# Optimization experiments

Measured on AMD Instinct MI355X. Metric: run time of the kernel, lower is better.

The kernel has to match this reference:

```python
import jax, jax.numpy as jnp
import numpy as np

D_IN = 1024
D_OUT = 1024
NUM_HEADS = 16
HEAD_DIM = D_OUT // NUM_HEADS


def setup_inputs() -> dict:
    key = jax.random.key(0)
    ks = jax.random.split(key, 6)
    s = 1.0 / np.sqrt(D_IN)
    inputs = jax.random.normal(ks[0], (4, 2048, D_IN), dtype=jnp.float32)
    Wq = jax.random.uniform(ks[1], (D_IN, D_OUT), jnp.float32, -s, s)
    Wk = jax.random.uniform(ks[2], (D_IN, D_OUT), jnp.float32, -s, s)
    Wv = jax.random.uniform(ks[3], (D_IN, D_OUT), jnp.float32, -s, s)
    so = 1.0 / np.sqrt(D_OUT)
    Wo = jax.random.uniform(ks[4], (D_OUT, D_OUT), jnp.float32, -so, so)
    bo = jax.random.uniform(ks[5], (D_OUT,), jnp.float32, -so, so)
    return {"inputs": inputs, "Wq": Wq, "Wk": Wk, "Wv": Wv, "Wo": Wo, "bo": bo}


def reference(inputs, Wq, Wk, Wv, Wo, bo):
    b, n, _ = inputs.shape
    # projections -> [b, h, n, d]
    def split_heads(x):
        return x.reshape(b, n, NUM_HEADS, HEAD_DIM).transpose(0, 2, 1, 3)
    q = split_heads(inputs @ Wq)
    k = split_heads(inputs @ Wk)
    v = split_heads(inputs @ Wv)
    scores = jnp.einsum('bhqd,bhkd->bhqk', q, k) / np.sqrt(HEAD_DIM).astype(np.float32)
    causal = jnp.tril(jnp.ones((n, n), dtype=bool))  # True = keep
    scores = jnp.where(causal, scores, -jnp.inf)
    weights = jax.nn.softmax(scores, axis=-1)
    ctx = jnp.einsum('bhqk,bhkd->bhqd', weights, v)
    ctx = ctx.transpose(0, 2, 1, 3).reshape(b, n, D_OUT)
    return ctx @ Wo + bo
```

## Files before the change

kernel.cpp:

```cpp
#include <hip/hip_runtime.h>

typedef unsigned short u16;
typedef unsigned int u32;
typedef __attribute__((ext_vector_type(8))) short short8;
typedef __attribute__((ext_vector_type(4))) float floatx4;
typedef __attribute__((ext_vector_type(4))) unsigned short ushort4_t;
typedef __attribute__((ext_vector_type(4))) float float4_t;
typedef __attribute__((ext_vector_type(2))) unsigned int uint2_t;


__device__ __forceinline__ u16 f2bf(float f) {
  unsigned u = __builtin_bit_cast(unsigned, f);
  u += 0x7FFFu + ((u >> 16) & 1u);
  return (u16)(u >> 16);
}

__device__ __forceinline__ u32 pack_bf2(float a, float b) {
  u32 ua = __builtin_bit_cast(u32, a) + 0x8000u;
  u32 ub = __builtin_bit_cast(u32, b) + 0x8000u;
  return __builtin_amdgcn_perm(ua, ub, 0x07060302u);
}

__device__ __forceinline__ void gload_lds16(const void* g, void* l) {
  __builtin_amdgcn_global_load_lds(
      (const __attribute__((address_space(1))) void*)g,
      (__attribute__((address_space(3))) void*)l, 16, 0, 0);
}


__global__ void cvt_x(const float* __restrict__ src, u16* __restrict__ dst) {
  int i = blockIdx.x * 256 + threadIdx.x;
  float4_t f = ((const float4_t*)src)[i];
  ushort4_t u;
  u.x = f2bf(f.x); u.y = f2bf(f.y); u.z = f2bf(f.z); u.w = f2bf(f.w);
  ((ushort4_t*)dst)[i] = u;
}

__global__ void transpose_cvt4(const float* __restrict__ wq, const float* __restrict__ wk,
                               const float* __restrict__ wv, const float* __restrict__ wo,
                               u16* __restrict__ qk, u16* __restrict__ vt,
                               u16* __restrict__ ot, float sc) {
  int i = blockIdx.x * 256 + threadIdx.x;
  int n = i >> 10, k = i & 1023;
  int which = blockIdx.y;
  const float* s = (which == 0) ? wq : (which == 1) ? wk : (which == 2) ? wv : wo;
  u16* d = (which == 0) ? qk : (which == 1) ? (qk + (1u << 20)) : (which == 2) ? vt : ot;
  float f = s[k * 1024 + n] * ((which == 0) ? sc : 1.f);
  d[i] = f2bf(f);
}

template <int MODE>
__global__ __launch_bounds__(256) void gemm_bt(
    const u16* __restrict__ A, const u16* __restrict__ Bt, void* __restrict__ Cv,
    const float* __restrict__ bias, int K, int lda, int ldb, int ldc) {
  __shared__ u16 As[128 * 32];
  __shared__ u16 Bs[128 * 32];
  const int tid = threadIdx.x;
  const int w = tid >> 6, l = tid & 63, quad = l >> 4, l16 = l & 15;
  const int wm = w >> 1, wn = w & 1;
  const size_t m0 = (size_t)blockIdx.y * 128, n0 = (size_t)blockIdx.x * 128;

  floatx4 acc[4][4];
  for (int i = 0; i < 4; ++i)
    for (int j = 0; j < 4; ++j) acc[i][j] = (floatx4){0.f, 0.f, 0.f, 0.f};

  for (int k0 = 0; k0 < K; k0 += 32) {
    __syncthreads();
    for (int i = 0; i < 2; ++i) {
      int c = i * 256 + tid;
      int row = c >> 2, off = (c & 3) * 8;
      gload_lds16(A + (m0 + row) * (size_t)lda + k0 + off, &As[c * 8]);
      gload_lds16(Bt + (n0 + row) * (size_t)ldb + k0 + off, &Bs[c * 8]);
    }
    __syncthreads();

    short8 a[4], bb[4];
    for (int im = 0; im < 4; ++im)
      a[im] = *(const short8*)&As[(wm * 64 + im * 16 + l16) * 32 + quad * 8];
    for (int in = 0; in < 4; ++in)
      bb[in] = *(const short8*)&Bs[(wn * 64 + in * 16 + l16) * 32 + quad * 8];
    for (int im = 0; im < 4; ++im)
      for (int in = 0; in < 4; ++in)
        acc[im][in] = __builtin_amdgcn_mfma_f32_16x16x32_bf16(a[im], bb[in], acc[im][in], 0, 0, 0);
  }

  for (int im = 0; im < 4; ++im)
    for (int in = 0; in < 4; ++in) {
      size_t r0 = m0 + wm * 64 + im * 16 + quad * 4;
      size_t col = n0 + wn * 64 + in * 16 + l16;
      float bv = (MODE == 1) ? bias[col] : 0.f;
      for (int r = 0; r < 4; ++r) {
        float val = acc[im][in][r] + bv;
        if (MODE == 0)
          ((u16*)Cv)[(r0 + r) * (size_t)ldc + col] = f2bf(val);
        else
          ((float*)Cv)[(r0 + r) * (size_t)ldc + col] = val;
      }
    }
}

__global__ __launch_bounds__(256) void flash_attn(
    const u16* __restrict__ QK, const u16* __restrict__ Vt, u16* __restrict__ ctx) {
  __shared__ u16 Ks[64 * 64];
  __shared__ u16 Vs[64 * 64];
  __shared__ u16 Ps[4 * 16 * 64];
  __shared__ float Ls[4 * 32];

  const int tid = threadIdx.x;
  const int w = tid >> 6, l = tid & 63, quad = l >> 4, l16 = l & 15;
  const int bh = blockIdx.x, qt = 15 - (int)blockIdx.y;
  const int b = bh >> 4, h = bh & 15;
  const int q0w = qt * 128 + w * 32;
  const int nkt = 2 * qt + 2;
  const int xr = (l16 & 7) << 4;

  short8 aq[2][2];
  for (int qf = 0; qf < 2; ++qf) {
    const size_t base = (size_t)(b * 2048 + q0w + qf * 16 + l16) * 2048 + h * 64 + quad * 8;
    aq[qf][0] = *(const short8*)(QK + base);
    aq[qf][1] = *(const short8*)(QK + base + 32);
  }

  floatx4 o[2][4];
  float lsum[2] = {0.f, 0.f};
  for (int qf = 0; qf < 2; ++qf)
    for (int df = 0; df < 4; ++df) o[qf][df] = (floatx4){0.f, 0.f, 0.f, 0.f};

  char* Psw = (char*)Ps + w * 2048;

  for (int kt = 0; kt < nkt; ++kt) {
    __syncthreads();
    for (int i = 0; i < 2; ++i) {
      int c = i * 256 + tid;
      int row = c >> 3, scol = ((c & 7) ^ (row & 7)) << 3;
      gload_lds16(QK + (size_t)(b * 2048 + kt * 64 + row) * 2048 + 1024 + h * 64 + scol,
                  &Ks[c * 8]);
      gload_lds16(Vt + (size_t)(h * 64 + row) * 8192 + b * 2048 + kt * 64 + scol,
                  &Vs[c * 8]);
    }
    __syncthreads();

    if (kt * 64 > q0w + 31) continue;
    const bool need_mask = (kt * 64 + 63) > q0w;

    short8 ka[4][2];
    for (int nf = 0; nf < 4; ++nf) {
      const char* kb = (const char*)Ks + (nf * 16 + l16) * 128;
      ka[nf][0] = *(const short8*)(kb + ((quad * 16) ^ xr));
      ka[nf][1] = *(const short8*)(kb + ((64 + quad * 16) ^ xr));
    }

    for (int qf = 0; qf < 2; ++qf) {
      floatx4 s[4];
      for (int nf = 0; nf < 4; ++nf) s[nf] = (floatx4){0.f, 0.f, 0.f, 0.f};
      for (int nf = 0; nf < 4; ++nf) {
        s[nf] = __builtin_amdgcn_mfma_f32_16x16x32_bf16(ka[nf][0], aq[qf][0], s[nf], 0, 0, 0);
        s[nf] = __builtin_amdgcn_mfma_f32_16x16x32_bf16(ka[nf][1], aq[qf][1], s[nf], 0, 0, 0);
      }
      if (need_mask) {
        int qpos = q0w + qf * 16 + l16;
        for (int nf = 0; nf < 4; ++nf)
          for (int r = 0; r < 4; ++r) {
            int kpos = kt * 64 + nf * 16 + quad * 4 + r;
            if (kpos > qpos) s[nf][r] = -1e30f;
          }
      }
      for (int nf = 0; nf < 4; ++nf) {
        float p0 = __builtin_amdgcn_exp2f(s[nf][0]);
        float p1 = __builtin_amdgcn_exp2f(s[nf][1]);
        float p2 = __builtin_amdgcn_exp2f(s[nf][2]);
        float p3 = __builtin_amdgcn_exp2f(s[nf][3]);
        lsum[qf] += (p0 + p1) + (p2 + p3);
        uint2_t pk;
        pk.x = pack_bf2(p1, p0);
        pk.y = pack_bf2(p3, p2);
        *(uint2_t*)(Psw + l16 * 128 + ((nf * 32 + quad * 8) ^ xr)) = pk;
      }
      for (int kk = 0; kk < 2; ++kk) {
        short8 ap = *(const short8*)(Psw + l16 * 128 + ((kk * 64 + quad * 16) ^ xr));
        for (int df = 0; df < 4; ++df) {
          const char* vb = (const char*)Vs + (df * 16 + l16) * 128;
          short8 bv = *(const short8*)(vb + ((kk * 64 + quad * 16) ^ xr));
          o[qf][df] = __builtin_amdgcn_mfma_f32_16x16x32_bf16(ap, bv, o[qf][df], 0, 0, 0);
        }
      }
    }
  }

  for (int qf = 0; qf < 2; ++qf) {
    float t = lsum[qf];
    t += __shfl_xor(t, 16, 64);
    t += __shfl_xor(t, 32, 64);
    if (l < 16) Ls[w * 32 + qf * 16 + l16] = __builtin_amdgcn_rcpf(t);
  }
  for (int qf = 0; qf < 2; ++qf) {
    floatx4 inv = *(const floatx4*)&Ls[w * 32 + qf * 16 + quad * 4];
    for (int df = 0; df < 4; ++df)
      for (int r = 0; r < 4; ++r) {
        float val = o[qf][df][r] * inv[r];
        size_t row = (size_t)(b * 2048 + q0w + qf * 16 + quad * 4 + r);
        ctx[row * 1024 + h * 64 + df * 16 + l16] = f2bf(val);
      }
  }
}


extern "C" void kernel_launch(void* const* d_in, const int* in_sizes, int n_in,
                              void* d_out, int out_size, void* d_ws, size_t ws_size,
                              hipStream_t stream) {
  const float* X  = (const float*)d_in[0];
  const float* Wq = (const float*)d_in[1];
  const float* Wk = (const float*)d_in[2];
  const float* Wv = (const float*)d_in[3];
  const float* Wo = (const float*)d_in[4];
  const float* bo = (const float*)d_in[5];

  char* ws = (char*)d_ws;
  u16* Xb   = (u16*)(ws);
  u16* WqkT = (u16*)(ws + (16u << 20));
  u16* WvT  = (u16*)(ws + (20u << 20));
  u16* WoT  = (u16*)(ws + (22u << 20));
  u16* QKb  = (u16*)(ws + (24u << 20));
  u16* Vt   = (u16*)(ws + (56u << 20));

  const float SC = 0.125f * 1.44269504088896340736f;

  cvt_x<<<8192, 256, 0, stream>>>(X, Xb);
  transpose_cvt4<<<dim3(4096, 4), 256, 0, stream>>>(Wq, Wk, Wv, Wo, WqkT, WvT, WoT, SC);

  gemm_bt<0><<<dim3(16, 64), 256, 0, stream>>>(Xb, WqkT, QKb, nullptr, 1024, 1024, 1024, 2048);
  gemm_bt<0><<<dim3(64, 8), 256, 0, stream>>>(WvT, Xb, Vt, nullptr, 1024, 1024, 1024, 8192);

  flash_attn<<<dim3(64, 16), 256, 0, stream>>>(QKb, Vt, Xb);

  gemm_bt<1><<<dim3(8, 64), 256, 0, stream>>>(Xb, WoT, (float*)d_out, bo, 1024, 1024, 1024, 1024);
}
```

Before: 287.5 us.

## Double-buffer LDS in GEMM and flash attention, tile weight transpose via shared memory

The GEMM and flash-attention kernels now use two LDS buffers, so the global-to-LDS load for the next K tile is issued before computing on the current one, with a single barrier per iteration. This overlaps memory latency with MFMA work. Flash attention also hoists all V fragment reads ahead of the qf loop and simplifies the masking test. The weight transpose now goes through a padded 64x65 shared tile so that both the global reads and writes are coalesced. The cost is twice the LDS footprint, which may lower occupancy, and more registers for the hoisted V fragments.

New measurement: 268.8 us. -6.5%, faster.

```diff
diff --git a/kernel.cpp b/kernel.cpp
--- a/kernel.cpp
+++ b/kernel.cpp
@@ -36,25 +36,34 @@
   ((ushort4_t*)dst)[i] = u;
 }
 
-__global__ void transpose_cvt4(const float* __restrict__ wq, const float* __restrict__ wk,
-                               const float* __restrict__ wv, const float* __restrict__ wo,
-                               u16* __restrict__ qk, u16* __restrict__ vt,
-                               u16* __restrict__ ot, float sc) {
-  int i = blockIdx.x * 256 + threadIdx.x;
-  int n = i >> 10, k = i & 1023;
-  int which = blockIdx.y;
+__global__ __launch_bounds__(256) void transpose_cvt4(
+    const float* __restrict__ wq, const float* __restrict__ wk,
+    const float* __restrict__ wv, const float* __restrict__ wo,
+    u16* __restrict__ qk, u16* __restrict__ vt, u16* __restrict__ ot, float sc) {
+  __shared__ float T[64][65];
+  const int which = blockIdx.z;
   const float* s = (which == 0) ? wq : (which == 1) ? wk : (which == 2) ? wv : wo;
   u16* d = (which == 0) ? qk : (which == 1) ? (qk + (1u << 20)) : (which == 2) ? vt : ot;
-  float f = s[k * 1024 + n] * ((which == 0) ? sc : 1.f);
-  d[i] = f2bf(f);
+  const float scale = (which == 0) ? sc : 1.f;
+  const int n0 = blockIdx.x * 64, k0 = blockIdx.y * 64;
+  const int c = threadIdx.x & 63, rg = threadIdx.x >> 6;
+  for (int i = 0; i < 16; ++i) {
+    int r = i * 4 + rg;
+    T[r][c] = s[(k0 + r) * 1024 + n0 + c];
+  }
+  __syncthreads();
+  for (int i = 0; i < 16; ++i) {
+    int r = i * 4 + rg;
+    d[(n0 + r) * 1024 + k0 + c] = f2bf(T[c][r] * scale);
+  }
 }
 
 template <int MODE>
 __global__ __launch_bounds__(256) void gemm_bt(
     const u16* __restrict__ A, const u16* __restrict__ Bt, void* __restrict__ Cv,
     const float* __restrict__ bias, int K, int lda, int ldb, int ldc) {
-  __shared__ u16 As[128 * 32];
-  __shared__ u16 Bs[128 * 32];
+  __shared__ u16 As[2][128 * 32];
+  __shared__ u16 Bs[2][128 * 32];
   const int tid = threadIdx.x;
   const int w = tid >> 6, l = tid & 63, quad = l >> 4, l16 = l & 15;
   const int wm = w >> 1, wn = w & 1;
@@ -64,24 +73,33 @@
   for (int i = 0; i < 4; ++i)
     for (int j = 0; j < 4; ++j) acc[i][j] = (floatx4){0.f, 0.f, 0.f, 0.f};
 
-  for (int k0 = 0; k0 < K; k0 += 32) {
-    __syncthreads();
+  auto stage = [&](int k0, int buf) {
     for (int i = 0; i < 2; ++i) {
       int c = i * 256 + tid;
       int row = c >> 2, off = (c & 3) * 8;
-      gload_lds16(A + (m0 + row) * (size_t)lda + k0 + off, &As[c * 8]);
-      gload_lds16(Bt + (n0 + row) * (size_t)ldb + k0 + off, &Bs[c * 8]);
-    }
-    __syncthreads();
+      gload_lds16(A + (m0 + row) * (size_t)lda + k0 + off, &As[buf][c * 8]);
+      gload_lds16(Bt + (n0 + row) * (size_t)ldb + k0 + off, &Bs[buf][c * 8]);
+    }
+  };
+
+  const int nk = K >> 5;
+  stage(0, 0);
+  __syncthreads();
+
+  for (int ki = 0; ki < nk; ++ki) {
+    const int buf = ki & 1;
+    if (ki + 1 < nk) stage((ki + 1) << 5, buf ^ 1);
 
     short8 a[4], bb[4];
     for (int im = 0; im < 4; ++im)
-      a[im] = *(const short8*)&As[(wm * 64 + im * 16 + l16) * 32 + quad * 8];
+      a[im] = *(const short8*)&As[buf][(wm * 64 + im * 16 + l16) * 32 + quad * 8];
     for (int in = 0; in < 4; ++in)
-      bb[in] = *(const short8*)&Bs[(wn * 64 + in * 16 + l16) * 32 + quad * 8];
+      bb[in] = *(const short8*)&Bs[buf][(wn * 64 + in * 16 + l16) * 32 + quad * 8];
     for (int im = 0; im < 4; ++im)
       for (int in = 0; in < 4; ++in)
         acc[im][in] = __builtin_amdgcn_mfma_f32_16x16x32_bf16(a[im], bb[in], acc[im][in], 0, 0, 0);
+
+    __syncthreads();
   }
 
   for (int im = 0; im < 4; ++im)
@@ -101,10 +119,10 @@
 
 __global__ __launch_bounds__(256) void flash_attn(
     const u16* __restrict__ QK, const u16* __restrict__ Vt, u16* __restrict__ ctx) {
-  __shared__ u16 Ks[64 * 64];
-  __shared__ u16 Vs[64 * 64];
+  __shared__ u16 Ks[2][64 * 64];
+  __shared__ u16 Vs[2][64 * 64];
   __shared__ u16 Ps[4 * 16 * 64];
-  __shared__ float Ls[4 * 32];
+  __shared__ float Ls[128];
 
   const int tid = threadIdx.x;
   const int w = tid >> 6, l = tid & 63, quad = l >> 4, l16 = l & 15;
@@ -112,7 +130,19 @@
   const int b = bh >> 4, h = bh & 15;
   const int q0w = qt * 128 + w * 32;
   const int nkt = 2 * qt + 2;
+  const int ktmax_w = (q0w + 31) >> 6;
   const int xr = (l16 & 7) << 4;
+
+  auto stage = [&](int kt, int buf) {
+    for (int i = 0; i < 2; ++i) {
+      int c = i * 256 + tid;
+      int row = c >> 3, scol = ((c & 7) ^ (row & 7)) << 3;
+      gload_lds16(QK + (size_t)(b * 2048 + kt * 64 + row) * 2048 + 1024 + h * 64 + scol,
+                  &Ks[buf][c * 8]);
+      gload_lds16(Vt + (size_t)(h * 64 + row) * 8192 + b * 2048 + kt * 64 + scol,
+                  &Vs[buf][c * 8]);
+    }
+  };
 
   short8 aq[2][2];
   for (int qf = 0; qf < 2; ++qf) {
@@ -128,63 +158,62 @@
 
   char* Psw = (char*)Ps + w * 2048;
 
+  stage(0, 0);
+  __syncthreads();
+
   for (int kt = 0; kt < nkt; ++kt) {
+    const int buf = kt & 1;
+    if (kt + 1 < nkt) stage(kt + 1, buf ^ 1);
+
+    if (kt <= ktmax_w) {
+      const bool need_mask = (kt == ktmax_w);
+
+      short8 ka[4][2], bv[4][2];
+      for (int nf = 0; nf < 4; ++nf) {
+        const char* kb = (const char*)&Ks[buf][0] + (nf * 16 + l16) * 128;
+        ka[nf][0] = *(const short8*)(kb + ((quad * 16) ^ xr));
+        ka[nf][1] = *(const short8*)(kb + ((64 + quad * 16) ^ xr));
+      }
+      for (int df = 0; df < 4; ++df) {
+        const char* vb = (const char*)&Vs[buf][0] + (df * 16 + l16) * 128;
+        bv[df][0] = *(const short8*)(vb + ((quad * 16) ^ xr));
+        bv[df][1] = *(const short8*)(vb + ((64 + quad * 16) ^ xr));
+      }
+
+      for (int qf = 0; qf < 2; ++qf) {
+        floatx4 s[4];
+        for (int nf = 0; nf < 4; ++nf) s[nf] = (floatx4){0.f, 0.f, 0.f, 0.f};
+        for (int nf = 0; nf < 4; ++nf) {
+          s[nf] = __builtin_amdgcn_mfma_f32_16x16x32_bf16(ka[nf][0], aq[qf][0], s[nf], 0, 0, 0);
+          s[nf] = __builtin_amdgcn_mfma_f32_16x16x32_bf16(ka[nf][1], aq[qf][1], s[nf], 0, 0, 0);
+        }
+        if (need_mask) {
+          int qpos = q0w + qf * 16 + l16;
+          for (int nf = 0; nf < 4; ++nf)
+            for (int r = 0; r < 4; ++r) {
+              int kpos = kt * 64 + nf * 16 + quad * 4 + r;
+              if (kpos > qpos) s[nf][r] = -1e30f;
+            }
+        }
+        for (int nf = 0; nf < 4; ++nf) {
+          float p0 = __builtin_amdgcn_exp2f(s[nf][0]);
+          float p1 = __builtin_amdgcn_exp2f(s[nf][1]);
+          float p2 = __builtin_amdgcn_exp2f(s[nf][2]);
+          float p3 = __builtin_amdgcn_exp2f(s[nf][3]);
+          lsum[qf] += (p0 + p1) + (p2 + p3);
+          uint2_t pk;
+          pk.x = pack_bf2(p1, p0);
+          pk.y = pack_bf2(p3, p2);
+          *(uint2_t*)(Psw + l16 * 128 + ((nf * 32 + quad * 8) ^ xr)) = pk;
+        }
+        for (int kk = 0; kk < 2; ++kk) {
+          short8 ap = *(const short8*)(Psw + l16 * 128 + ((kk * 64 + quad * 16) ^ xr));
+          for (int df = 0; df < 4; ++df)
+            o[qf][df] = __builtin_amdgcn_mfma_f32_16x16x32_bf16(ap, bv[df][kk], o[qf][df], 0, 0, 0);
+        }
+      }
+    }
     __syncthreads();
-    for (int i = 0; i < 2; ++i) {
-      int c = i * 256 + tid;
-      int row = c >> 3, scol = ((c & 7) ^ (row & 7)) << 3;
-      gload_lds16(QK + (size_t)(b * 2048 + kt * 64 + row) * 2048 + 1024 + h * 64 + scol,
-                  &Ks[c * 8]);
-      gload_lds16(Vt + (size_t)(h * 64 + row) * 8192 + b * 2048 + kt * 64 + scol,
-                  &Vs[c * 8]);
-    }
-    __syncthreads();
-
-    if (kt * 64 > q0w + 31) continue;
-    const bool need_mask = (kt * 64 + 63) > q0w;
-
-    short8 ka[4][2];
-    for (int nf = 0; nf < 4; ++nf) {
-      const char* kb = (const char*)Ks + (nf * 16 + l16) * 128;
-      ka[nf][0] = *(const short8*)(kb + ((quad * 16) ^ xr));
-      ka[nf][1] = *(const short8*)(kb + ((64 + quad * 16) ^ xr));
-    }
-
-    for (int qf = 0; qf < 2; ++qf) {
-      floatx4 s[4];
-      for (int nf = 0; nf < 4; ++nf) s[nf] = (floatx4){0.f, 0.f, 0.f, 0.f};
-      for (int nf = 0; nf < 4; ++nf) {
-        s[nf] = __builtin_amdgcn_mfma_f32_16x16x32_bf16(ka[nf][0], aq[qf][0], s[nf], 0, 0, 0);
-        s[nf] = __builtin_amdgcn_mfma_f32_16x16x32_bf16(ka[nf][1], aq[qf][1], s[nf], 0, 0, 0);
-      }
-      if (need_mask) {
-        int qpos = q0w + qf * 16 + l16;
-        for (int nf = 0; nf < 4; ++nf)
-          for (int r = 0; r < 4; ++r) {
-            int kpos = kt * 64 + nf * 16 + quad * 4 + r;
-            if (kpos > qpos) s[nf][r] = -1e30f;
-          }
-      }
-      for (int nf = 0; nf < 4; ++nf) {
-        float p0 = __builtin_amdgcn_exp2f(s[nf][0]);
-        float p1 = __builtin_amdgcn_exp2f(s[nf][1]);
-        float p2 = __builtin_amdgcn_exp2f(s[nf][2]);
-        float p3 = __builtin_amdgcn_exp2f(s[nf][3]);
-        lsum[qf] += (p0 + p1) + (p2 + p3);
-        uint2_t pk;
-        pk.x = pack_bf2(p1, p0);
-        pk.y = pack_bf2(p3, p2);
-        *(uint2_t*)(Psw + l16 * 128 + ((nf * 32 + quad * 8) ^ xr)) = pk;
-      }
-      for (int kk = 0; kk < 2; ++kk) {
-        short8 ap = *(const short8*)(Psw + l16 * 128 + ((kk * 64 + quad * 16) ^ xr));
-        for (int df = 0; df < 4; ++df) {
-          const char* vb = (const char*)Vs + (df * 16 + l16) * 128;
-          short8 bv = *(const short8*)(vb + ((kk * 64 + quad * 16) ^ xr));
-          o[qf][df] = __builtin_amdgcn_mfma_f32_16x16x32_bf16(ap, bv, o[qf][df], 0, 0, 0);
-        }
-      }
-    }
   }
 
   for (int qf = 0; qf < 2; ++qf) {
@@ -226,7 +255,7 @@
   const float SC = 0.125f * 1.44269504088896340736f;
 
   cvt_x<<<8192, 256, 0, stream>>>(X, Xb);
-  transpose_cvt4<<<dim3(4096, 4), 256, 0, stream>>>(Wq, Wk, Wv, Wo, WqkT, WvT, WoT, SC);
+  transpose_cvt4<<<dim3(16, 16, 4), 256, 0, stream>>>(Wq, Wk, Wv, Wo, WqkT, WvT, WoT, SC);
 
   gemm_bt<0><<<dim3(16, 64), 256, 0, stream>>>(Xb, WqkT, QKb, nullptr, 1024, 1024, 1024, 2048);
   gemm_bt<0><<<dim3(64, 8), 256, 0, stream>>>(WvT, Xb, Vt, nullptr, 1024, 1024, 1024, 8192);
```
